# Performance work log

Measured on AMD Instinct MI355X. Metric: run time of the kernel, lower is better.

Reference implementation:

```python
import jax, jax.numpy as jnp
import numpy as np

B, S, NC, ND, V = 16, 512, 10000, 10000, 128


def _rn(k, shape, scale=0.05):
    return jax.random.normal(k, shape, dtype=jnp.float32) * scale


def setup_inputs() -> dict:
    key = jax.random.key(0)
    ks = jax.random.split(key, 24)
    inp = {
        'c_seq': jax.random.randint(ks[0], (B, S), 0, NC),
        'd_seq': jax.random.randint(ks[1], (B, S), 0, ND),
        'r_seq': jax.random.uniform(ks[2], (B, S), dtype=jnp.float32),
        # embeddings / vectors
        'D1_w': _rn(ks[3], (ND, 1)),
        'D2_w': _rn(ks[4], (ND, V)),
        'v_r': _rn(ks[5], (V,)),
        'v_beta': _rn(ks[6], (V,)),
        # GRU (torch layout: gates ordered r,z,n; W_ih [3V,2V], W_hh [3V,V])
        'W_ih': _rn(ks[7], (3 * V, 2 * V)),
        'W_hh': _rn(ks[8], (3 * V, V)),
        'b_ih': jnp.zeros((3 * V,), jnp.float32),
        'b_hh': jnp.zeros((3 * V,), jnp.float32),
        # linear_1: V -> V -> V -> 1 (weights stored [in, out])
        'm1_W1': _rn(ks[9], (V, V)), 'm1_b1': jnp.zeros((V,), jnp.float32),
        'm1_W2': _rn(ks[10], (V, V)), 'm1_b2': jnp.zeros((V,), jnp.float32),
        'm1_W3': _rn(ks[11], (V, 1)), 'm1_b3': jnp.zeros((1,), jnp.float32),
        # linear_2: 3V -> V -> V -> 1
        'm2_W1': _rn(ks[12], (3 * V, V)), 'm2_b1': jnp.zeros((V,), jnp.float32),
        'm2_W2': _rn(ks[13], (V, V)), 'm2_b2': jnp.zeros((V,), jnp.float32),
        'm2_W3': _rn(ks[14], (V, 1)), 'm2_b3': jnp.zeros((1,), jnp.float32),
    }
    return inp


def _mlp(x, W1, b1, W2, b2, W3, b3):
    h = jax.nn.relu(x @ W1 + b1)
    h = jax.nn.relu(h @ W2 + b2)
    return h @ W3 + b3


def _gru_seq(x, W_ih, W_hh, b_ih, b_hh):
    # x: [B,S,2V] -> h_seq [B,S,V]; torch GRU gate order r,z,n
    xp = x @ W_ih.T + b_ih  # [B,S,3V]

    def step(h, xt):
        hp = h @ W_hh.T + b_hh
        xr, xz, xn = jnp.split(xt, 3, axis=-1)
        hr, hz, hn = jnp.split(hp, 3, axis=-1)
        r = jax.nn.sigmoid(xr + hr)
        z = jax.nn.sigmoid(xz + hz)
        n = jnp.tanh(xn + r * hn)
        h_new = (1.0 - z) * n + z * h
        return h_new, h_new

    h0 = jnp.zeros((x.shape[0], W_hh.shape[1]), x.dtype)
    _, hs = jax.lax.scan(step, h0, jnp.swapaxes(xp, 0, 1))  # [S,B,V]
    return jnp.swapaxes(hs, 0, 1)


def reference(c_seq, d_seq, r_seq, D1_w, D2_w, v_r, v_beta,
              W_ih, W_hh, b_ih, b_hh,
              m1_W1, m1_b1, m1_W2, m1_b2, m1_W3, m1_b3,
              m2_W1, m2_b1, m2_W2, m2_b2, m2_W3, m2_b3):
    v_d_seq = D2_w[d_seq]                     # [B,S,V]
    v_r_seq = r_seq[..., None] * v_r          # [B,S,V]

    h_seq = _gru_seq(jnp.concatenate([v_d_seq, v_r_seq], axis=-1),
                     W_ih, W_hh, b_ih, b_hh)  # [B,S,V]
    alpha_seq = _mlp(h_seq, m1_W1, m1_b1, m1_W2, m1_b2, m1_W3, m1_b3)[..., 0]  # [B,S]

    bidx = jnp.arange(c_seq.shape[0])

    def step(C, ins):
        c_t, vd_t, vr_t = ins                 # [B], [B,V], [B,V]
        beta_prev = C[bidx, c_t]              # gather: [B]
        v_beta_prev = beta_prev[:, None] * v_beta  # [B,V]
        new_c = _mlp(jnp.concatenate([v_beta_prev, vd_t, vr_t], axis=-1),
                     m2_W1, m2_b1, m2_W2, m2_b2, m2_W3, m2_b3)[:, 0]  # [B]
        C = C.at[bidx, c_t].set(new_c)        # scatter
        return C, (C, new_c)

    C0 = jnp.zeros((c_seq.shape[0], NC), jnp.float32)
    _, (C_seq, beta_seq) = jax.lax.scan(
        step, C0,
        (jnp.swapaxes(c_seq, 0, 1), jnp.swapaxes(v_d_seq, 0, 1), jnp.swapaxes(v_r_seq, 0, 1)))
    C_seq = jnp.swapaxes(C_seq, 0, 1)[..., None]   # [B,S,NC,1]
    beta_seq = jnp.swapaxes(beta_seq, 0, 1)        # [B,S]

    gamma_seq = D1_w[d_seq][..., 0]                # [B,S]
    return (alpha_seq, beta_seq, gamma_seq, h_seq, C_seq)
```

## Files before the change

### kernel.cpp

```cpp
#include <hip/hip_runtime.h>

#define Bq   16
#define Sq   512
#define Vq   128
#define NCq  10000

typedef __attribute__((ext_vector_type(8))) short short8v;
typedef __attribute__((ext_vector_type(4))) float f32x4;

#define OFF_P1B_U  3145728u
#define OFF_WTIH   2097152u
#define OFF_WVRIH  2146304u
#define OFF_WVR1   2146688u
#define OFF_WVB    2146816u
#define OFF_PO     2146944u

#define PLN 136
#define PLSZ (16*PLN+8)

__device__ __forceinline__ unsigned short f2bf(float x) {
    unsigned u = __builtin_bit_cast(unsigned, x);
    unsigned r = (u + 0x7fffu + ((u >> 16) & 1u)) >> 16;
    return (unsigned short)r;
}
__device__ __forceinline__ float bfhi(unsigned u) {
    return __builtin_bit_cast(float, u << 16);
}
__device__ __forceinline__ float bflo(unsigned u) {
    return __builtin_bit_cast(float, u & 0xffff0000u);
}
__device__ __forceinline__ void barrier_lgkm() {
    asm volatile("s_waitcnt lgkmcnt(0)" ::: "memory");
    __builtin_amdgcn_sched_barrier(0);
    __builtin_amdgcn_s_barrier();
    __builtin_amdgcn_sched_barrier(0);
}
__device__ __forceinline__ void wait_vm0() {
    asm volatile("s_waitcnt vmcnt(0)" ::: "memory");
    __builtin_amdgcn_sched_barrier(0);
}
__device__ __forceinline__ void gload_lds16(const void* g, void* l) {
    __builtin_amdgcn_global_load_lds(
        (const __attribute__((address_space(1))) unsigned int*)g,
        (__attribute__((address_space(3))) unsigned int*)l, 16, 0, 0);
}

__global__ __launch_bounds__(256) void k0_prep(
    const int* __restrict__ c_seq, const int* __restrict__ d_seq,
    const float* __restrict__ D1_w,
    const float* __restrict__ W_ih,
    const float* __restrict__ v_r, const float* __restrict__ v_beta,
    const float* __restrict__ m2W1,
    float* __restrict__ ws, float* __restrict__ gamma_out)
{
    const int blk = blockIdx.x, tid = threadIdx.x;

    if (blk < 128) {
        float* WTIH = ws + OFF_WTIH;
        int base = blk * 384;
        for (int i = tid; i < 384; i += 256) {
            int e = base + i;
            int k = e / 384, g = e % 384;
            WTIH[e] = W_ih[g * 256 + k];
        }
    } else if (blk == 128) {
        float* WVRIH = ws + OFF_WVRIH;
        float* WVR1  = ws + OFF_WVR1;
        float* WVB   = ws + OFF_WVB;
        for (int g = tid; g < 384; g += 256) {
            float a = 0.f;
            for (int k = 0; k < 128; ++k) a = fmaf(v_r[k], W_ih[g * 256 + 128 + k], a);
            WVRIH[g] = a;
        }
        if (tid < 128) {
            float a = 0.f, b = 0.f;
            for (int k = 0; k < 128; ++k) {
                a = fmaf(v_r[k],    m2W1[(256 + k) * 128 + tid], a);
                b = fmaf(v_beta[k], m2W1[k * 128 + tid],         b);
            }
            WVR1[tid] = a; WVB[tid] = b;
        }
    } else if (blk < 145) {
        const int b = blk - 129;
        __shared__ int cs[Sq];
        for (int i = tid; i < Sq; i += 256) cs[i] = c_seq[b * Sq + i];
        __syncthreads();
        int* PO = (int*)(ws + OFF_PO);
        for (int t = tid; t < Sq; t += 256) {
            int c = cs[t];
            int po = -1;
            for (int u = t - 1; u >= 0; --u) if (cs[u] == c) { po = u; break; }
            PO[t * 16 + b] = po;
        }
    } else {
        const int b = blk - 145;
        for (int s = tid; s < Sq; s += 256)
            gamma_out[b * Sq + s] = D1_w[d_seq[b * Sq + s]];
    }
}

__global__ __launch_bounds__(256) void k1_gemm(
    const int* __restrict__ d_seq, const float* __restrict__ D2_w,
    const float* __restrict__ m2W1,
    const float* __restrict__ b_ih, const float* __restrict__ b_hh,
    const float* __restrict__ r_seq, const float* __restrict__ m2b1,
    float* __restrict__ ws)
{
    __shared__ float As[64 * 128];
    __shared__ float Bs[128 * 64];
    const int blk = blockIdx.x, tid = threadIdx.x;
    const int nc = blk & 7;
    const int m0 = (blk >> 3) * 64;
    const float* WTIH = ws + OFF_WTIH;

    const float4* D2v = (const float4*)D2_w;
    for (int e = tid; e < 2048; e += 256) {
        int r = e >> 5, q = e & 31;
        int d = d_seq[m0 + r];
        *(float4*)&As[r * 128 + 4 * q] = D2v[d * 32 + q];
    }
    for (int e = tid; e < 2048; e += 256) {
        int k = e >> 4, q = e & 15;
        float4 v;
        if (nc < 6) v = *(const float4*)&WTIH[k * 384 + nc * 64 + 4 * q];
        else        v = *(const float4*)&m2W1[(128 + k) * 128 + (nc - 6) * 64 + 4 * q];
        *(float4*)&Bs[k * 64 + 4 * q] = v;
    }
    __syncthreads();

    const int tx = tid & 15, ty = tid >> 4;
    const int c0 = 4 * tx, r0 = 4 * ty;
    float acc[4][4];
#pragma unroll
    for (int i = 0; i < 4; ++i)
#pragma unroll
        for (int j = 0; j < 4; ++j) acc[i][j] = 0.f;

    for (int k = 0; k < 128; ++k) {
        float4 bv = *(const float4*)&Bs[k * 64 + c0];
#pragma unroll
        for (int i = 0; i < 4; ++i) {
            float a = As[(r0 + i) * 128 + k];
            acc[i][0] = fmaf(a, bv.x, acc[i][0]);
            acc[i][1] = fmaf(a, bv.y, acc[i][1]);
            acc[i][2] = fmaf(a, bv.z, acc[i][2]);
            acc[i][3] = fmaf(a, bv.w, acc[i][3]);
        }
    }

    float rsv[4];
#pragma unroll
    for (int i = 0; i < 4; ++i) rsv[i] = r_seq[m0 + r0 + i];

    if (nc < 6) {
        const int grow0 = nc * 64 + c0;
        float4 bi  = *(const float4*)&b_ih[grow0];
        float4 wv4 = *(const float4*)&(ws + OFF_WVRIH)[grow0];
        float4 bh4 = make_float4(0.f, 0.f, 0.f, 0.f);
        if (nc < 4) bh4 = *(const float4*)&b_hh[grow0];
        unsigned short* XPB = (unsigned short*)ws;
        const int r4 = grow0 >> 2;
#pragma unroll
        for (int i = 0; i < 4; ++i) {
            int row = m0 + r0 + i;
            int t = row & 511, bb = row >> 9;
            float vx = acc[i][0] + bi.x + bh4.x + rsv[i] * wv4.x;
            float vy = acc[i][1] + bi.y + bh4.y + rsv[i] * wv4.y;
            float vz = acc[i][2] + bi.z + bh4.z + rsv[i] * wv4.z;
            float vw = acc[i][3] + bi.w + bh4.w + rsv[i] * wv4.w;
            uint2 p;
            p.x = (unsigned)f2bf(vx) | ((unsigned)f2bf(vy) << 16);
            p.y = (unsigned)f2bf(vz) | ((unsigned)f2bf(vw) << 16);
            *(uint2*)&XPB[((size_t)((bb >> 2) * 512 + t)) * 1536 + r4 * 16 + (bb & 3) * 4] = p;
        }
    } else {
        const int j0 = (nc - 6) * 64 + c0;
        float4 b1v = *(const float4*)&m2b1[j0];
        float4 wr1 = *(const float4*)&(ws + OFF_WVR1)[j0];
        unsigned short* P1B = (unsigned short*)ws + OFF_P1B_U;
#pragma unroll
        for (int i = 0; i < 4; ++i) {
            int row = m0 + r0 + i;
            int t = row & 511, bb = row >> 9;
            float vx = acc[i][0] + b1v.x + rsv[i] * wr1.x;
            float vy = acc[i][1] + b1v.y + rsv[i] * wr1.y;
            float vz = acc[i][2] + b1v.z + rsv[i] * wr1.z;
            float vw = acc[i][3] + b1v.w + rsv[i] * wr1.w;
            uint2 p;
            p.x = (unsigned)f2bf(vx) | ((unsigned)f2bf(vy) << 16);
            p.y = (unsigned)f2bf(vz) | ((unsigned)f2bf(vw) << 16);
            *(uint2*)&P1B[((size_t)(t * 16 + bb)) * 128 + j0] = p;
        }
    }
}

__global__ __launch_bounds__(512, 1) void k2_scan(
    const float* __restrict__ W_hh, const float* __restrict__ b_hh,
    const float* __restrict__ m2W2, const float* __restrict__ m2b2,
    const float* __restrict__ m2W3, const float* __restrict__ m2b3,
    float* __restrict__ ws,
    float* __restrict__ hseq_out, float* __restrict__ beta_out)
{
    __shared__ __align__(16) unsigned char smem[57984];
    const int tid = threadIdx.x;
    const int l = tid & 63, wv = tid >> 6;
    const int qq = l >> 4, cb = l & 15;
    const int bgid = blockIdx.x;

    if (bgid < 4) {
        unsigned short* hP  = (unsigned short*)smem;
        unsigned short* xch = (unsigned short*)(smem + 8736);
        const unsigned short* XPB = (const unsigned short*)ws;

        short8v aH0[4], aH1[4], aH2[4];
#pragma unroll
        for (int kf = 0; kf < 4; ++kf) {
            const int kb = kf * 32 + qq * 8;
            const float* w0 = W_hh + (0 * 128 + 16 * wv + cb) * 128 + kb;
            const float* w1 = W_hh + (1 * 128 + 16 * wv + cb) * 128 + kb;
            const float* w2 = W_hh + (2 * 128 + 16 * wv + cb) * 128 + kb;
            short8v h0, h1, h2;
#pragma unroll
            for (int e = 0; e < 8; ++e) {
                h0[e] = (short)f2bf(w0[e]);
                h1[e] = (short)f2bf(w1[e]);
                h2[e] = (short)f2bf(w2[e]);
            }
            aH0[kf] = h0; aH1[kf] = h1; aH2[kf] = h2;
        }
        float bhn[4];
        *(float4*)bhn = *(const float4*)&b_hh[256 + 16 * wv + 4 * qq];

        float* hp = hseq_out + ((size_t)((bgid * 4 + (cb & 3)) * 512)) * 128 + 16 * wv + 4 * qq;
        float hold[4] = {0.f, 0.f, 0.f, 0.f};
        for (int i = tid; i < 2 * PLSZ; i += 512) hP[i] = 0;
#pragma unroll
        for (int rr = 0; rr < 3; ++rr)
            gload_lds16(XPB + (size_t)(bgid * 512) * 1536 + (rr * 512 + tid) * 8,
                        xch + (rr * 512 + tid) * 8);
        __syncthreads();

        for (int t = 0; t < 512; ++t) {
            const int r = t & 7;
            if (r < 3 && t < 504) {
                const unsigned short* src =
                    XPB + (size_t)(bgid * 512 + ((t >> 3) + 1) * 8) * 1536 + (r * 512 + tid) * 8;
                unsigned short* dst = xch + (((t >> 3) + 1) & 1) * 12288 + (r * 512 + tid) * 8;
                gload_lds16(src, dst);
            }
            const unsigned short* xc =
                xch + ((t >> 3) & 1) * 12288 + r * 1536 + (4 * wv + qq) * 16 + (cb & 3) * 4;
            uint2 u0 = *(const uint2*)(xc);
            uint2 u1 = *(const uint2*)(xc + 512);
            uint2 u2 = *(const uint2*)(xc + 1024);
            float pf0[4] = {bfhi(u0.x), bflo(u0.x), bfhi(u0.y), bflo(u0.y)};
            float pf1[4] = {bfhi(u1.x), bflo(u1.x), bfhi(u1.y), bflo(u1.y)};
            float pf2[4] = {bfhi(u2.x), bflo(u2.x), bfhi(u2.y), bflo(u2.y)};

            const unsigned short* HI = hP + (t & 1) * PLSZ;
            unsigned short* HIn = hP + ((t + 1) & 1) * PLSZ;

            f32x4 C0a = {0.f,0.f,0.f,0.f}, C1a = {0.f,0.f,0.f,0.f}, C2a = {0.f,0.f,0.f,0.f};
            f32x4 C0b = {0.f,0.f,0.f,0.f}, C1b = {0.f,0.f,0.f,0.f}, C2b = {0.f,0.f,0.f,0.f};
            {
                short8v B0 = *(const short8v*)(HI + cb * PLN + 0 * 32 + qq * 8);
                short8v B1 = *(const short8v*)(HI + cb * PLN + 1 * 32 + qq * 8);
                short8v B2 = *(const short8v*)(HI + cb * PLN + 2 * 32 + qq * 8);
                short8v B3 = *(const short8v*)(HI + cb * PLN + 3 * 32 + qq * 8);
                C0a = __builtin_amdgcn_mfma_f32_16x16x32_bf16(aH0[0], B0, C0a, 0, 0, 0);
                C1a = __builtin_amdgcn_mfma_f32_16x16x32_bf16(aH1[0], B0, C1a, 0, 0, 0);
                C2a = __builtin_amdgcn_mfma_f32_16x16x32_bf16(aH2[0], B0, C2a, 0, 0, 0);
                C0b = __builtin_amdgcn_mfma_f32_16x16x32_bf16(aH0[1], B1, C0b, 0, 0, 0);
                C1b = __builtin_amdgcn_mfma_f32_16x16x32_bf16(aH1[1], B1, C1b, 0, 0, 0);
                C2b = __builtin_amdgcn_mfma_f32_16x16x32_bf16(aH2[1], B1, C2b, 0, 0, 0);
                C0a = __builtin_amdgcn_mfma_f32_16x16x32_bf16(aH0[2], B2, C0a, 0, 0, 0);
                C1a = __builtin_amdgcn_mfma_f32_16x16x32_bf16(aH1[2], B2, C1a, 0, 0, 0);
                C2a = __builtin_amdgcn_mfma_f32_16x16x32_bf16(aH2[2], B2, C2a, 0, 0, 0);
                C0b = __builtin_amdgcn_mfma_f32_16x16x32_bf16(aH0[3], B3, C0b, 0, 0, 0);
                C1b = __builtin_amdgcn_mfma_f32_16x16x32_bf16(aH1[3], B3, C1b, 0, 0, 0);
                C2b = __builtin_amdgcn_mfma_f32_16x16x32_bf16(aH2[3], B3, C2b, 0, 0, 0);
            }
            float hnew[4];
#pragma unroll
            for (int i = 0; i < 4; ++i) {
                float pr = (C0a[i] + C0b[i]) + pf0[i];
                float pz = (C1a[i] + C1b[i]) + pf1[i];
                float rr2 = __builtin_amdgcn_rcpf(1.f + __expf(-pr));
                float z = __builtin_amdgcn_rcpf(1.f + __expf(-pz));
                float hn = (C2a[i] + C2b[i]) + bhn[i];
                float npre = fmaf(rr2, hn, pf2[i]);
                float e2 = __expf(-2.f * fabsf(npre));
                float n = copysignf((1.f - e2) * __builtin_amdgcn_rcpf(1.f + e2), npre);
                float hv = fmaf(z, hold[i] - n, n);
                hold[i] = hv;
                hnew[i] = hv;
            }
            if (cb < 4) {
                *(float4*)hp = make_float4(hnew[0], hnew[1], hnew[2], hnew[3]);
                uint2 hw;
                hw.x = (unsigned)f2bf(hnew[0]) | ((unsigned)f2bf(hnew[1]) << 16);
                hw.y = (unsigned)f2bf(hnew[2]) | ((unsigned)f2bf(hnew[3]) << 16);
                *(uint2*)(HIn + cb * PLN + 16 * wv + 4 * qq) = hw;
            }
            hp += 128;
            if (r == 7) wait_vm0();
            barrier_lgkm();
        }
    } else {
        const int bq = bgid - 4;
        float* bhL = (float*)smem;
        int*   poT = (int*)(smem + 8192);
        unsigned short* h1P = (unsigned short*)(smem + 16384);
        float* redT = (float*)(smem + 20752);
        unsigned short* pch = (unsigned short*)(smem + 20880);
        const unsigned short* P1B = (const unsigned short*)ws + OFF_P1B_U;
        const int* POg = (const int*)(ws + OFF_PO);

        short8v aH[4];
#pragma unroll
        for (int kf = 0; kf < 4; ++kf) {
            short8v hi;
#pragma unroll
            for (int e = 0; e < 8; ++e)
                hi[e] = (short)f2bf(m2W2[(kf * 32 + qq * 8 + e) * 128 + 16 * wv + cb]);
            aH[kf] = hi;
        }
        float w3C[4], b2C[4];
        *(float4*)w3C = *(const float4*)&m2W3[16 * wv + 4 * qq];
        *(float4*)b2C = *(const float4*)&m2b2[16 * wv + 4 * qq];
        const float b3v = m2b3[0];

        const bool pa = (tid < 128);
        const int bb2 = tid & 3, j4 = (tid >> 2) & 31;
        float wvb[4] = {0.f, 0.f, 0.f, 0.f};
        if (pa) *(float4*)wvb = *(const float4*)&(ws + OFF_WVB)[j4 * 4];
        float btap = 0.f;

        for (int i = tid; i < 2048; i += 512)
            poT[i] = POg[(i >> 2) * 16 + 4 * bq + (i & 3)];
        for (int i = tid; i < PLSZ; i += 512) h1P[i] = 0;
        gload_lds16(P1B + (size_t)(wv * 16 + 4 * bq) * 128 + l * 8,
                    pch + wv * 512 + l * 8);
        __syncthreads();

        for (int t = 0; t < 512; ++t) {
            const int r = t & 7;
            if (pa) {
                if (t > 0) {
                    float4 ra = *(const float4*)&redT[bb2 * 8];
                    float4 rb = *(const float4*)&redT[bb2 * 8 + 4];
                    btap = ((ra.x + ra.y) + (ra.z + ra.w)) +
                           ((rb.x + rb.y) + (rb.z + rb.w)) + b3v;
                    if (j4 == 0) bhL[bb2 * 512 + (t - 1)] = btap;
                }
                int po = poT[t * 4 + bb2];
                float bp = (po == t - 1) ? btap : ((po >= 0) ? bhL[bb2 * 512 + po] : 0.f);
                const unsigned short* pc =
                    pch + ((t >> 3) & 1) * 4096 + r * 512 + bb2 * 128 + j4 * 4;
                uint2 u = *(const uint2*)pc;
                float h0 = fmaxf(0.f, fmaf(bp, wvb[0], bfhi(u.x)));
                float h1 = fmaxf(0.f, fmaf(bp, wvb[1], bflo(u.x)));
                float h2 = fmaxf(0.f, fmaf(bp, wvb[2], bfhi(u.y)));
                float h3 = fmaxf(0.f, fmaf(bp, wvb[3], bflo(u.y)));
                uint2 hw;
                hw.x = (unsigned)f2bf(h0) | ((unsigned)f2bf(h1) << 16);
                hw.y = (unsigned)f2bf(h2) | ((unsigned)f2bf(h3) << 16);
                *(uint2*)(h1P + bb2 * PLN + j4 * 4) = hw;
            }
            if (r == 0 && t < 504) {
                const unsigned short* src =
                    P1B + (size_t)((t + 8 + wv) * 16 + 4 * bq) * 128 + l * 8;
                unsigned short* dst = pch + (((t >> 3) + 1) & 1) * 4096 + wv * 512 + l * 8;
                gload_lds16(src, dst);
            }
            barrier_lgkm();

            f32x4 Ca = {0.f, 0.f, 0.f, 0.f}, Cb = {0.f, 0.f, 0.f, 0.f};
            {
                short8v B0 = *(const short8v*)(h1P + cb * PLN + 0 * 32 + qq * 8);
                short8v B1 = *(const short8v*)(h1P + cb * PLN + 1 * 32 + qq * 8);
                short8v B2 = *(const short8v*)(h1P + cb * PLN + 2 * 32 + qq * 8);
                short8v B3 = *(const short8v*)(h1P + cb * PLN + 3 * 32 + qq * 8);
                Ca = __builtin_amdgcn_mfma_f32_16x16x32_bf16(aH[0], B0, Ca, 0, 0, 0);
                Cb = __builtin_amdgcn_mfma_f32_16x16x32_bf16(aH[1], B1, Cb, 0, 0, 0);
                Ca = __builtin_amdgcn_mfma_f32_16x16x32_bf16(aH[2], B2, Ca, 0, 0, 0);
                Cb = __builtin_amdgcn_mfma_f32_16x16x32_bf16(aH[3], B3, Cb, 0, 0, 0);
            }
            float part = 0.f;
#pragma unroll
            for (int i = 0; i < 4; ++i)
                part = fmaf(fmaxf(0.f, (Ca[i] + Cb[i]) + b2C[i]), w3C[i], part);
            part += __shfl_xor(part, 16);
            part += __shfl_xor(part, 32);
            if (qq == 0 && cb < 4) redT[cb * 8 + wv] = part;
            if (r == 7) wait_vm0();
            barrier_lgkm();
        }
        if (pa) {
            float4 ra = *(const float4*)&redT[bb2 * 8];
            float4 rb = *(const float4*)&redT[bb2 * 8 + 4];
            float bta = ((ra.x + ra.y) + (ra.z + ra.w)) +
                        ((rb.x + rb.y) + (rb.z + rb.w)) + b3v;
            if (j4 == 0) bhL[bb2 * 512 + 511] = bta;
        }
        __syncthreads();
        for (int i = tid; i < 2048; i += 512)
            beta_out[(4 * bq + (i >> 9)) * 512 + (i & 511)] = bhL[i];
    }
}

__global__ __launch_bounds__(256) void k2b_fill(
    const int* __restrict__ c_seq, const float* __restrict__ beta_in,
    float* __restrict__ C_out)
{
    __shared__ int   scs[Sq];
    __shared__ float sbt[Sq];
    const int bid = blockIdx.x, tid = threadIdx.x;
    const int b = bid / 40, rem = bid % 40;
    const int chunk = rem >> 2, q = rem & 3;

    for (int i = tid; i < Sq; i += 256) {
        scs[i] = c_seq[b * Sq + i];
        sbt[i] = beta_in[b * Sq + i];
    }
    __syncthreads();

    const int c0 = chunk * 1024 + tid * 4;
    if (c0 >= NCq) return;

    float cur0 = 0.f, cur1 = 0.f, cur2 = 0.f, cur3 = 0.f;
    const int tlo = q * 128, thi = tlo + 128;
    float* base = C_out + (size_t)b * Sq * NCq + c0;

    for (int t = 0; t < tlo; ++t) {
        int ct = scs[t] - c0; float bv = sbt[t];
        cur0 = (ct == 0) ? bv : cur0;
        cur1 = (ct == 1) ? bv : cur1;
        cur2 = (ct == 2) ? bv : cur2;
        cur3 = (ct == 3) ? bv : cur3;
    }
    for (int t = tlo; t < thi; ++t) {
        int ct = scs[t] - c0; float bv = sbt[t];
        cur0 = (ct == 0) ? bv : cur0;
        cur1 = (ct == 1) ? bv : cur1;
        cur2 = (ct == 2) ? bv : cur2;
        cur3 = (ct == 3) ? bv : cur3;
        *(float4*)(base + (size_t)t * NCq) = make_float4(cur0, cur1, cur2, cur3);
    }
}

__global__ __launch_bounds__(256) void k3_alpha(
    const float* __restrict__ hseq,
    const float* __restrict__ W1, const float* __restrict__ b1,
    const float* __restrict__ W2, const float* __restrict__ b2,
    const float* __restrict__ W3, const float* __restrict__ b3,
    float* __restrict__ alpha_out)
{
    __shared__ float Hs[32 * 128];
    __shared__ float T1[32 * 128];
    __shared__ float red[4][16];
    const int blk = blockIdx.x, tid = threadIdx.x;
    const int row0 = blk * 32;

    for (int e = tid; e < 1024; e += 256) {
        int r = e >> 5, q = e & 31;
        *(float4*)&Hs[r * 128 + 4 * q] =
            *(const float4*)&hseq[(size_t)(row0 + r) * 128 + 4 * q];
    }
    __syncthreads();

    const int j = tid & 127, rh = tid >> 7;
    const float b1j = b1[j], b2j = b2[j], w3j = W3[j];
    float acc[16];
#pragma unroll
    for (int r = 0; r < 16; ++r) acc[r] = b1j;
    for (int k = 0; k < 128; ++k) {
        float w = W1[k * 128 + j];
#pragma unroll
        for (int r = 0; r < 16; ++r)
            acc[r] = fmaf(Hs[(rh * 16 + r) * 128 + k], w, acc[r]);
    }
#pragma unroll
    for (int r = 0; r < 16; ++r) {
        acc[r] = fmaxf(acc[r], 0.f);
        T1[(rh * 16 + r) * 128 + j] = acc[r];
    }
    __syncthreads();
    float acc2[16];
#pragma unroll
    for (int r = 0; r < 16; ++r) acc2[r] = b2j;
    for (int k = 0; k < 128; ++k) {
        float w = W2[k * 128 + j];
#pragma unroll
        for (int r = 0; r < 16; ++r)
            acc2[r] = fmaf(T1[(rh * 16 + r) * 128 + k], w, acc2[r]);
    }
#pragma unroll
    for (int r = 0; r < 16; ++r) {
        float p = fmaxf(acc2[r], 0.f) * w3j;
#pragma unroll
        for (int off = 1; off < 64; off <<= 1) p += __shfl_xor(p, off);
        if ((tid & 63) == 0) red[tid >> 6][r] = p;
    }
    __syncthreads();
    if (tid < 32) {
        int rr = tid & 15, g = tid >> 4;
        alpha_out[row0 + g * 16 + rr] = red[2 * g][rr] + red[2 * g + 1][rr] + b3[0];
    }
}

extern "C" void kernel_launch(void* const* d_in, const int* in_sizes, int n_in,
                              void* d_out, int out_size, void* d_ws, size_t ws_size,
                              hipStream_t stream) {
    const int*   c_seq = (const int*)d_in[0];
    const int*   d_seq = (const int*)d_in[1];
    const float* r_seq = (const float*)d_in[2];
    const float* D1_w  = (const float*)d_in[3];
    const float* D2_w  = (const float*)d_in[4];
    const float* v_r   = (const float*)d_in[5];
    const float* v_b   = (const float*)d_in[6];
    const float* W_ih  = (const float*)d_in[7];
    const float* W_hh  = (const float*)d_in[8];
    const float* b_ih  = (const float*)d_in[9];
    const float* b_hh  = (const float*)d_in[10];
    const float* m1W1  = (const float*)d_in[11];
    const float* m1b1  = (const float*)d_in[12];
    const float* m1W2  = (const float*)d_in[13];
    const float* m1b2  = (const float*)d_in[14];
    const float* m1W3  = (const float*)d_in[15];
    const float* m1b3  = (const float*)d_in[16];
    const float* m2W1  = (const float*)d_in[17];
    const float* m2b1  = (const float*)d_in[18];
    const float* m2W2  = (const float*)d_in[19];
    const float* m2b2  = (const float*)d_in[20];
    const float* m2W3  = (const float*)d_in[21];
    const float* m2b3  = (const float*)d_in[22];

    float* out   = (float*)d_out;
    float* alpha = out;
    float* beta  = out + 8192;
    float* gamma = out + 16384;
    float* hseq  = out + 24576;
    float* Cseq  = out + 1073152;
    float* ws    = (float*)d_ws;

    hipLaunchKernelGGL(k0_prep, dim3(161), dim3(256), 0, stream,
                       c_seq, d_seq, D1_w, W_ih, v_r, v_b, m2W1, ws, gamma);
    hipLaunchKernelGGL(k1_gemm, dim3(1024), dim3(256), 0, stream,
                       d_seq, D2_w, m2W1, b_ih, b_hh, r_seq, m2b1, ws);
    hipLaunchKernelGGL(k2_scan, dim3(8), dim3(512), 0, stream,
                       W_hh, b_hh, m2W2, m2b2, m2W3, m2b3, ws, hseq, beta);
    hipLaunchKernelGGL(k2b_fill, dim3(640), dim3(256), 0, stream,
                       c_seq, beta, Cseq);
    hipLaunchKernelGGL(k3_alpha, dim3(256), dim3(256), 0, stream,
                       hseq, m1W1, m1b1, m1W2, m1b2, m1W3, m1b3, alpha);
}
```

Measured before the change: 630.4 us.

## Stage fp32 precomputed inputs per step with rolling prefetch in scan kernels

Precomputed GRU input projections and MLP layer-1 partials are now stored in fp32 rather than bf16. The scan kernels prefetch them one timestep at a time into a 4-slot LDS ring, three steps ahead, replacing the 8-step batched double buffer. The same change folds biases and input projections into the MFMA accumulator initial values, uses exp2-based sigmoid/tanh and the hardware packed bf16 convert, and prefetches the scatter-index (po) lookups one step ahead to shorten the serial per-step chain. In exchange it moves twice the bytes for the precomputed buffers, issues a load and a partial vmcnt wait every step, and uses a larger workspace.

```diff
diff --git a/kernel.cpp b/kernel.cpp
--- a/kernel.cpp
+++ b/kernel.cpp
@@ -8,26 +8,21 @@
 typedef __attribute__((ext_vector_type(8))) short short8v;
 typedef __attribute__((ext_vector_type(4))) float f32x4;
 
-#define OFF_P1B_U  3145728u
-#define OFF_WTIH   2097152u
-#define OFF_WVRIH  2146304u
-#define OFF_WVR1   2146688u
-#define OFF_WVB    2146816u
-#define OFF_PO     2146944u
+#define OFF_XPF    0u
+#define OFF_P1F    3145728u
+#define OFF_WTIH   4194304u
+#define OFF_WVRIH  4243456u
+#define OFF_WVR1   4243840u
+#define OFF_WVB    4243968u
+#define OFF_PO     4244096u
 
 #define PLN 136
 #define PLSZ (16*PLN+8)
 
-__device__ __forceinline__ unsigned short f2bf(float x) {
-    unsigned u = __builtin_bit_cast(unsigned, x);
-    unsigned r = (u + 0x7fffu + ((u >> 16) & 1u)) >> 16;
-    return (unsigned short)r;
-}
-__device__ __forceinline__ float bfhi(unsigned u) {
-    return __builtin_bit_cast(float, u << 16);
-}
-__device__ __forceinline__ float bflo(unsigned u) {
-    return __builtin_bit_cast(float, u & 0xffff0000u);
+__device__ __forceinline__ unsigned cvt_pk_bf16(float a, float b) {
+    unsigned r;
+    asm("v_cvt_pk_bf16_f32 %0, %1, %2" : "=v"(r) : "v"(a), "v"(b));
+    return r;
 }
 __device__ __forceinline__ void barrier_lgkm() {
     asm volatile("s_waitcnt lgkmcnt(0)" ::: "memory");
@@ -35,8 +30,12 @@
     __builtin_amdgcn_s_barrier();
     __builtin_amdgcn_sched_barrier(0);
 }
-__device__ __forceinline__ void wait_vm0() {
-    asm volatile("s_waitcnt vmcnt(0)" ::: "memory");
+__device__ __forceinline__ void wait_vm4() {
+    asm volatile("s_waitcnt vmcnt(4)" ::: "memory");
+    __builtin_amdgcn_sched_barrier(0);
+}
+__device__ __forceinline__ void wait_vm2() {
+    asm volatile("s_waitcnt vmcnt(2)" ::: "memory");
     __builtin_amdgcn_sched_barrier(0);
 }
 __device__ __forceinline__ void gload_lds16(const void* g, void* l) {
@@ -158,38 +157,34 @@
         float4 wv4 = *(const float4*)&(ws + OFF_WVRIH)[grow0];
         float4 bh4 = make_float4(0.f, 0.f, 0.f, 0.f);
         if (nc < 4) bh4 = *(const float4*)&b_hh[grow0];
-        unsigned short* XPB = (unsigned short*)ws;
+        float* XPF = ws + OFF_XPF;
         const int r4 = grow0 >> 2;
 #pragma unroll
         for (int i = 0; i < 4; ++i) {
             int row = m0 + r0 + i;
             int t = row & 511, bb = row >> 9;
-            float vx = acc[i][0] + bi.x + bh4.x + rsv[i] * wv4.x;
-            float vy = acc[i][1] + bi.y + bh4.y + rsv[i] * wv4.y;
-            float vz = acc[i][2] + bi.z + bh4.z + rsv[i] * wv4.z;
-            float vw = acc[i][3] + bi.w + bh4.w + rsv[i] * wv4.w;
-            uint2 p;
-            p.x = (unsigned)f2bf(vx) | ((unsigned)f2bf(vy) << 16);
-            p.y = (unsigned)f2bf(vz) | ((unsigned)f2bf(vw) << 16);
-            *(uint2*)&XPB[((size_t)((bb >> 2) * 512 + t)) * 1536 + r4 * 16 + (bb & 3) * 4] = p;
+            float4 v;
+            v.x = acc[i][0] + bi.x + bh4.x + rsv[i] * wv4.x;
+            v.y = acc[i][1] + bi.y + bh4.y + rsv[i] * wv4.y;
+            v.z = acc[i][2] + bi.z + bh4.z + rsv[i] * wv4.z;
+            v.w = acc[i][3] + bi.w + bh4.w + rsv[i] * wv4.w;
+            *(float4*)&XPF[((size_t)((bb >> 2) * 512 + t)) * 1536 + r4 * 16 + (bb & 3) * 4] = v;
         }
     } else {
         const int j0 = (nc - 6) * 64 + c0;
         float4 b1v = *(const float4*)&m2b1[j0];
         float4 wr1 = *(const float4*)&(ws + OFF_WVR1)[j0];
-        unsigned short* P1B = (unsigned short*)ws + OFF_P1B_U;
+        float* P1F = ws + OFF_P1F;
 #pragma unroll
         for (int i = 0; i < 4; ++i) {
             int row = m0 + r0 + i;
             int t = row & 511, bb = row >> 9;
-            float vx = acc[i][0] + b1v.x + rsv[i] * wr1.x;
-            float vy = acc[i][1] + b1v.y + rsv[i] * wr1.y;
-            float vz = acc[i][2] + b1v.z + rsv[i] * wr1.z;
-            float vw = acc[i][3] + b1v.w + rsv[i] * wr1.w;
-            uint2 p;
-            p.x = (unsigned)f2bf(vx) | ((unsigned)f2bf(vy) << 16);
-            p.y = (unsigned)f2bf(vz) | ((unsigned)f2bf(vw) << 16);
-            *(uint2*)&P1B[((size_t)(t * 16 + bb)) * 128 + j0] = p;
+            float4 v;
+            v.x = acc[i][0] + b1v.x + rsv[i] * wr1.x;
+            v.y = acc[i][1] + b1v.y + rsv[i] * wr1.y;
+            v.z = acc[i][2] + b1v.z + rsv[i] * wr1.z;
+            v.w = acc[i][3] + b1v.w + rsv[i] * wr1.w;
+            *(float4*)&P1F[((size_t)(t * 16 + bb)) * 128 + j0] = v;
         }
     }
 }
@@ -201,7 +196,7 @@
     float* __restrict__ ws,
     float* __restrict__ hseq_out, float* __restrict__ beta_out)
 {
-    __shared__ __align__(16) unsigned char smem[57984];
+    __shared__ __align__(16) unsigned char smem[41504];
     const int tid = threadIdx.x;
     const int l = tid & 63, wv = tid >> 6;
     const int qq = l >> 4, cb = l & 15;
@@ -209,8 +204,8 @@
 
     if (bgid < 4) {
         unsigned short* hP  = (unsigned short*)smem;
-        unsigned short* xch = (unsigned short*)(smem + 8736);
-        const unsigned short* XPB = (const unsigned short*)ws;
+        unsigned char*  xsl = smem + 8736;
+        const float* XPF = ws + OFF_XPF;
 
         short8v aH0[4], aH1[4], aH2[4];
 #pragma unroll
@@ -222,45 +217,46 @@
             short8v h0, h1, h2;
 #pragma unroll
             for (int e = 0; e < 8; ++e) {
-                h0[e] = (short)f2bf(w0[e]);
-                h1[e] = (short)f2bf(w1[e]);
-                h2[e] = (short)f2bf(w2[e]);
+                unsigned u0 = __builtin_bit_cast(unsigned, w0[e]);
+                unsigned u1 = __builtin_bit_cast(unsigned, w1[e]);
+                unsigned u2 = __builtin_bit_cast(unsigned, w2[e]);
+                h0[e] = (short)((u0 + 0x7fffu + ((u0 >> 16) & 1u)) >> 16);
+                h1[e] = (short)((u1 + 0x7fffu + ((u1 >> 16) & 1u)) >> 16);
+                h2[e] = (short)((u2 + 0x7fffu + ((u2 >> 16) & 1u)) >> 16);
             }
             aH0[kf] = h0; aH1[kf] = h1; aH2[kf] = h2;
         }
-        float bhn[4];
-        *(float4*)bhn = *(const float4*)&b_hh[256 + 16 * wv + 4 * qq];
+        f32x4 bhn4;
+        {
+            float4 t4 = *(const float4*)&b_hh[256 + 16 * wv + 4 * qq];
+            bhn4[0] = t4.x; bhn4[1] = t4.y; bhn4[2] = t4.z; bhn4[3] = t4.w;
+        }
 
         float* hp = hseq_out + ((size_t)((bgid * 4 + (cb & 3)) * 512)) * 128 + 16 * wv + 4 * qq;
         float hold[4] = {0.f, 0.f, 0.f, 0.f};
         for (int i = tid; i < 2 * PLSZ; i += 512) hP[i] = 0;
 #pragma unroll
-        for (int rr = 0; rr < 3; ++rr)
-            gload_lds16(XPB + (size_t)(bgid * 512) * 1536 + (rr * 512 + tid) * 8,
-                        xch + (rr * 512 + tid) * 8);
+        for (int s = 0; s < 3; ++s)
+            gload_lds16(XPF + ((size_t)(bgid * 512 + s)) * 1536 + tid * 4,
+                        xsl + s * 8192 + tid * 16);
         __syncthreads();
 
+        const float NL2E = -1.44269504f, L2E2 = 2.88539008f;
         for (int t = 0; t < 512; ++t) {
-            const int r = t & 7;
-            if (r < 3 && t < 504) {
-                const unsigned short* src =
-                    XPB + (size_t)(bgid * 512 + ((t >> 3) + 1) * 8) * 1536 + (r * 512 + tid) * 8;
-                unsigned short* dst = xch + (((t >> 3) + 1) & 1) * 12288 + (r * 512 + tid) * 8;
-                gload_lds16(src, dst);
-            }
-            const unsigned short* xc =
-                xch + ((t >> 3) & 1) * 12288 + r * 1536 + (4 * wv + qq) * 16 + (cb & 3) * 4;
-            uint2 u0 = *(const uint2*)(xc);
-            uint2 u1 = *(const uint2*)(xc + 512);
-            uint2 u2 = *(const uint2*)(xc + 1024);
-            float pf0[4] = {bfhi(u0.x), bflo(u0.x), bfhi(u0.y), bflo(u0.y)};
-            float pf1[4] = {bfhi(u1.x), bflo(u1.x), bfhi(u1.y), bflo(u1.y)};
-            float pf2[4] = {bfhi(u2.x), bflo(u2.x), bfhi(u2.y), bflo(u2.y)};
+            if (t < 509)
+                gload_lds16(XPF + ((size_t)(bgid * 512 + t + 3)) * 1536 + tid * 4,
+                            xsl + ((t + 3) & 3) * 8192 + tid * 16);
+
+            const float* xc = (const float*)(xsl + (t & 3) * 8192) +
+                              (4 * wv + qq) * 16 + (cb & 3) * 4;
+            f32x4 px0 = *(const f32x4*)(xc);
+            f32x4 px1 = *(const f32x4*)(xc + 512);
+            f32x4 px2 = *(const f32x4*)(xc + 1024);
 
             const unsigned short* HI = hP + (t & 1) * PLSZ;
             unsigned short* HIn = hP + ((t + 1) & 1) * PLSZ;
 
-            f32x4 C0a = {0.f,0.f,0.f,0.f}, C1a = {0.f,0.f,0.f,0.f}, C2a = {0.f,0.f,0.f,0.f};
+            f32x4 C0a = px0, C1a = px1, C2a = bhn4;
             f32x4 C0b = {0.f,0.f,0.f,0.f}, C1b = {0.f,0.f,0.f,0.f}, C2b = {0.f,0.f,0.f,0.f};
             {
                 short8v B0 = *(const short8v*)(HI + cb * PLN + 0 * 32 + qq * 8);
@@ -283,14 +279,13 @@
             float hnew[4];
 #pragma unroll
             for (int i = 0; i < 4; ++i) {
-                float pr = (C0a[i] + C0b[i]) + pf0[i];
-                float pz = (C1a[i] + C1b[i]) + pf1[i];
-                float rr2 = __builtin_amdgcn_rcpf(1.f + __expf(-pr));
-                float z = __builtin_amdgcn_rcpf(1.f + __expf(-pz));
-                float hn = (C2a[i] + C2b[i]) + bhn[i];
-                float npre = fmaf(rr2, hn, pf2[i]);
-                float e2 = __expf(-2.f * fabsf(npre));
-                float n = copysignf((1.f - e2) * __builtin_amdgcn_rcpf(1.f + e2), npre);
+                float pr = C0a[i] + C0b[i];
+                float pz = C1a[i] + C1b[i];
+                float hn = C2a[i] + C2b[i];
+                float r = __builtin_amdgcn_rcpf(1.f + __builtin_amdgcn_exp2f(pr * NL2E));
+                float z = __builtin_amdgcn_rcpf(1.f + __builtin_amdgcn_exp2f(pz * NL2E));
+                float npre = fmaf(r, hn, px2[i]);
+                float n = fmaf(-2.f, __builtin_amdgcn_rcpf(1.f + __builtin_amdgcn_exp2f(npre * L2E2)), 1.f);
                 float hv = fmaf(z, hold[i] - n, n);
                 hold[i] = hv;
                 hnew[i] = hv;
@@ -298,22 +293,21 @@
             if (cb < 4) {
                 *(float4*)hp = make_float4(hnew[0], hnew[1], hnew[2], hnew[3]);
                 uint2 hw;
-                hw.x = (unsigned)f2bf(hnew[0]) | ((unsigned)f2bf(hnew[1]) << 16);
-                hw.y = (unsigned)f2bf(hnew[2]) | ((unsigned)f2bf(hnew[3]) << 16);
+                hw.x = cvt_pk_bf16(hnew[0], hnew[1]);
+                hw.y = cvt_pk_bf16(hnew[2], hnew[3]);
                 *(uint2*)(HIn + cb * PLN + 16 * wv + 4 * qq) = hw;
             }
             hp += 128;
-            if (r == 7) wait_vm0();
+            wait_vm4();
             barrier_lgkm();
         }
     } else {
         const int bq = bgid - 4;
         float* bhL = (float*)smem;
-        int*   poT = (int*)(smem + 8192);
-        unsigned short* h1P = (unsigned short*)(smem + 16384);
-        float* redT = (float*)(smem + 20752);
-        unsigned short* pch = (unsigned short*)(smem + 20880);
-        const unsigned short* P1B = (const unsigned short*)ws + OFF_P1B_U;
+        unsigned short* h1P = (unsigned short*)(smem + 8192);
+        float* redT = (float*)(smem + 12560);
+        unsigned char* psl = smem + 12688;
+        const float* P1F = ws + OFF_P1F;
         const int* POg = (const int*)(ws + OFF_PO);
 
         short8v aH[4];
@@ -321,30 +315,40 @@
         for (int kf = 0; kf < 4; ++kf) {
             short8v hi;
 #pragma unroll
-            for (int e = 0; e < 8; ++e)
-                hi[e] = (short)f2bf(m2W2[(kf * 32 + qq * 8 + e) * 128 + 16 * wv + cb]);
+            for (int e = 0; e < 8; ++e) {
+                unsigned u = __builtin_bit_cast(unsigned,
+                    m2W2[(kf * 32 + qq * 8 + e) * 128 + 16 * wv + cb]);
+                hi[e] = (short)((u + 0x7fffu + ((u >> 16) & 1u)) >> 16);
+            }
             aH[kf] = hi;
         }
-        float w3C[4], b2C[4];
+        float w3C[4];
+        f32x4 b2C4;
         *(float4*)w3C = *(const float4*)&m2W3[16 * wv + 4 * qq];
-        *(float4*)b2C = *(const float4*)&m2b2[16 * wv + 4 * qq];
+        {
+            float4 t4 = *(const float4*)&m2b2[16 * wv + 4 * qq];
+            b2C4[0] = t4.x; b2C4[1] = t4.y; b2C4[2] = t4.z; b2C4[3] = t4.w;
+        }
         const float b3v = m2b3[0];
 
         const bool pa = (tid < 128);
         const int bb2 = tid & 3, j4 = (tid >> 2) & 31;
         float wvb[4] = {0.f, 0.f, 0.f, 0.f};
-        if (pa) *(float4*)wvb = *(const float4*)&(ws + OFF_WVB)[j4 * 4];
-        float btap = 0.f;
-
-        for (int i = tid; i < 2048; i += 512)
-            poT[i] = POg[(i >> 2) * 16 + 4 * bq + (i & 3)];
+        int poCur = -1, poNxt = -1;
+        float bpPre = 0.f, btap = 0.f;
+        if (pa) {
+            *(float4*)wvb = *(const float4*)&(ws + OFF_WVB)[j4 * 4];
+            poCur = POg[0 * 16 + 4 * bq + bb2];
+            poNxt = POg[1 * 16 + 4 * bq + bb2];
+#pragma unroll
+            for (int s = 0; s < 3; ++s)
+                gload_lds16(P1F + ((size_t)(s * 16 + 4 * bq)) * 128 + tid * 4,
+                            psl + s * 2048 + tid * 16);
+        }
         for (int i = tid; i < PLSZ; i += 512) h1P[i] = 0;
-        gload_lds16(P1B + (size_t)(wv * 16 + 4 * bq) * 128 + l * 8,
-                    pch + wv * 512 + l * 8);
         __syncthreads();
 
         for (int t = 0; t < 512; ++t) {
-            const int r = t & 7;
             if (pa) {
                 if (t > 0) {
                     float4 ra = *(const float4*)&redT[bb2 * 8];
@@ -353,29 +357,31 @@
                            ((rb.x + rb.y) + (rb.z + rb.w)) + b3v;
                     if (j4 == 0) bhL[bb2 * 512 + (t - 1)] = btap;
                 }
-                int po = poT[t * 4 + bb2];
-                float bp = (po == t - 1) ? btap : ((po >= 0) ? bhL[bb2 * 512 + po] : 0.f);
-                const unsigned short* pc =
-                    pch + ((t >> 3) & 1) * 4096 + r * 512 + bb2 * 128 + j4 * 4;
-                uint2 u = *(const uint2*)pc;
-                float h0 = fmaxf(0.f, fmaf(bp, wvb[0], bfhi(u.x)));
-                float h1 = fmaxf(0.f, fmaf(bp, wvb[1], bflo(u.x)));
-                float h2 = fmaxf(0.f, fmaf(bp, wvb[2], bfhi(u.y)));
-                float h3 = fmaxf(0.f, fmaf(bp, wvb[3], bflo(u.y)));
+                int po = poCur;
+                float bp = (po == t - 1) ? btap : bpPre;
+                const float* pc = (const float*)(psl + (t & 3) * 2048) + bb2 * 128 + j4 * 4;
+                f32x4 p1 = *(const f32x4*)pc;
+                float h0 = fmaxf(0.f, fmaf(bp, wvb[0], p1[0]));
+                float h1 = fmaxf(0.f, fmaf(bp, wvb[1], p1[1]));
+                float h2 = fmaxf(0.f, fmaf(bp, wvb[2], p1[2]));
+                float h3 = fmaxf(0.f, fmaf(bp, wvb[3], p1[3]));
                 uint2 hw;
-                hw.x = (unsigned)f2bf(h0) | ((unsigned)f2bf(h1) << 16);
-                hw.y = (unsigned)f2bf(h2) | ((unsigned)f2bf(h3) << 16);
+                hw.x = cvt_pk_bf16(h0, h1);
+                hw.y = cvt_pk_bf16(h2, h3);
                 *(uint2*)(h1P + bb2 * PLN + j4 * 4) = hw;
-            }
-            if (r == 0 && t < 504) {
-                const unsigned short* src =
-                    P1B + (size_t)((t + 8 + wv) * 16 + 4 * bq) * 128 + l * 8;
-                unsigned short* dst = pch + (((t >> 3) + 1) & 1) * 4096 + wv * 512 + l * 8;
-                gload_lds16(src, dst);
+                if (t < 509)
+                    gload_lds16(P1F + ((size_t)((t + 3) * 16 + 4 * bq)) * 128 + tid * 4,
+                                psl + ((t + 3) & 3) * 2048 + tid * 16);
             }
             barrier_lgkm();
 
-            f32x4 Ca = {0.f, 0.f, 0.f, 0.f}, Cb = {0.f, 0.f, 0.f, 0.f};
+            if (pa) {
+                bpPre = 0.f;
+                if (poNxt >= 0 && poNxt < t) bpPre = bhL[bb2 * 512 + poNxt];
+                poCur = poNxt;
+                if (t < 510) poNxt = POg[(t + 2) * 16 + 4 * bq + bb2];
+            }
+            f32x4 Ca = b2C4, Cb = {0.f, 0.f, 0.f, 0.f};
             {
                 short8v B0 = *(const short8v*)(h1P + cb * PLN + 0 * 32 + qq * 8);
                 short8v B1 = *(const short8v*)(h1P + cb * PLN + 1 * 32 + qq * 8);
@@ -389,11 +395,11 @@
             float part = 0.f;
 #pragma unroll
             for (int i = 0; i < 4; ++i)
-                part = fmaf(fmaxf(0.f, (Ca[i] + Cb[i]) + b2C[i]), w3C[i], part);
+                part = fmaf(fmaxf(0.f, Ca[i] + Cb[i]), w3C[i], part);
             part += __shfl_xor(part, 16);
             part += __shfl_xor(part, 32);
             if (qq == 0 && cb < 4) redT[cb * 8 + wv] = part;
-            if (r == 7) wait_vm0();
+            wait_vm2();
             barrier_lgkm();
         }
         if (pa) {
```

Result: no change. 618.8 us (-1.8%).
